# Kernel tuning notes

Hardware: AMD Instinct MI355X
Metric: run time of the kernel (lower is better)

## Reference

```python
import jax, jax.numpy as jnp
import numpy as np
import math

BATCH, T, D_INNER, D_STATE, K = 2, 1024, 1024, 16, 4


def setup_inputs() -> dict:
    key = jax.random.key(0)
    ks = jax.random.split(key, 6)
    x = jax.random.normal(ks[0], (BATCH, T, D_INNER), jnp.float32)
    conv_w = jax.random.normal(ks[1], (D_INNER, 1, K), jnp.float32) * (1.0 / math.sqrt(K))
    conv_b = jax.random.normal(ks[2], (D_INNER,), jnp.float32) * 0.02
    x_proj_w = jax.random.normal(ks[3], (2 * D_STATE, D_INNER), jnp.float32) * (1.0 / math.sqrt(D_INNER))
    dt_proj_w = jax.random.normal(ks[4], (D_INNER, D_STATE), jnp.float32) * (1.0 / math.sqrt(D_STATE))
    dt_proj_b = jax.random.uniform(ks[5], (D_INNER,), jnp.float32, minval=math.log(0.001), maxval=math.log(0.1))
    D = jnp.ones((D_INNER,), jnp.float32)
    return {"x": x, "conv_w": conv_w, "conv_b": conv_b, "x_proj_w": x_proj_w,
            "dt_proj_w": dt_proj_w, "dt_proj_b": dt_proj_b, "D": D}


def _ssm_forward(x, conv_w, conv_b, x_proj_w, dt_proj_w, dt_proj_b, D):
    B_batch, T_len, d_inner = x.shape
    d_state = dt_proj_w.shape[1]
    k = conv_w.shape[-1]
    # Causal depthwise conv1d: torch pads (k-1) both sides then slices [:T] == left-pad (k-1), VALID.
    xp = jnp.pad(x.transpose(0, 2, 1), ((0, 0), (0, 0), (k - 1, 0)))  # (B, d_inner, T+k-1)
    xc = jax.lax.conv_general_dilated(
        xp, conv_w, window_strides=(1,), padding='VALID',
        dimension_numbers=('NCH', 'OIH', 'NCH'), feature_group_count=d_inner)
    xc = xc + conv_b[None, :, None]
    xc = jax.nn.silu(xc).transpose(0, 2, 1)  # (B, T, d_inner)

    proj = jnp.einsum('btd,pd->btp', xc, x_proj_w)  # (B, T, 2*d_state)
    B_ssm, C_ssm = jnp.split(proj, 2, axis=-1)      # each (B, T, d_state)

    # NOTE: original applies softplus twice (once in forward, once in selective_scan).
    dt = jax.nn.softplus(jnp.einsum('bts,ds->btd', B_ssm, dt_proj_w) + dt_proj_b)
    dt = jax.nn.softplus(dt)  # (B, T, d_inner)

    # A = -exp(log(arange(1..d_state))) = -[1..d_state], same for every d_inner channel.
    A = -jnp.arange(1, d_state + 1, dtype=x.dtype)  # (d_state,)

    dA = jnp.exp(dt[..., None] * A)                                  # (B, T, d_inner, d_state)
    dBx = dt[..., None] * B_ssm[:, :, None, :] * xc[..., None]       # (B, T, d_inner, d_state)

    flat = d_inner * d_state
    EPS = 1e-38
    log_dA = jnp.log(jnp.clip(dA, EPS)).reshape(B_batch, T_len, flat)
    log_dBx = jnp.log(jnp.clip(dBx, EPS)).reshape(B_batch, T_len, flat)

    # parallel_scan_log: h_t = exp(cumsum(log_dA) + logcumsumexp(log_dBx - cumsum(log_dA)))
    a_star = jnp.cumsum(log_dA, axis=1)
    h = jnp.exp(a_star + jax.lax.cumlogsumexp(log_dBx - a_star, axis=1))
    h = h.reshape(B_batch, T_len, d_inner, d_state)

    y = jnp.einsum('bts,btds->btd', C_ssm, h) + D * xc
    return y


def reference(x, conv_w, conv_b, x_proj_w, dt_proj_w, dt_proj_b, D):
    return _ssm_forward(x, conv_w, conv_b, x_proj_w, dt_proj_w, dt_proj_b, D)
```

## Files before the change

### kernel.cpp

```cpp
#include <hip/hip_runtime.h>

#define BATCH 2
#define T_LEN 1024
#define D_IN  1024
#define D_ST  16
#define CHUNKS 32
#define CLEN  32
#define DTILE 64
#define NTILES 1024
#define NRPAIR 1024
#define NCHAIN4 8192

struct ABts {
    float row0[D_IN];
    float row1[D_IN];
    alignas(16) float Bsh[2][D_ST];
};
struct Tile {
    float dt[CLEN][DTILE];
    float xc[CLEN][DTILE];
    alignas(16) float B[CLEN][D_ST];
    alignas(16) float C[CLEN][D_ST];
};

__device__ __forceinline__ float softplus_f(float x) {
    return fmaxf(x, 0.0f) + __logf(1.0f + __expf(-fabsf(x)));
}
__device__ __forceinline__ void ld4(float* dst, const float4* src) {
    float4 v = *src; dst[0] = v.x; dst[1] = v.y; dst[2] = v.z; dst[3] = v.w;
}

__device__ __forceinline__ void phase_ab(
    ABts& ab, int rpair, int tid,
    const float* __restrict__ x, const float* __restrict__ cw,
    const float* __restrict__ cb, const float* __restrict__ xpw,
    const float* __restrict__ dtw, const float* __restrict__ dtb,
    float* __restrict__ xcg, float* __restrict__ dtp,
    float* __restrict__ Bss, float* __restrict__ Css)
{
    const int r0g = rpair * 2;
    const int b   = r0g >> 10;
    const int t   = r0g & 1023;
    const int d0  = tid * 4;
    const float* xb = x + (size_t)b * T_LEN * D_IN + d0;
    const float4 z4 = {0,0,0,0};
    float xm3[4], xm2[4], xm1[4], x00[4], xp1[4], wv[16], bb[4];
    { float4 v = (t>=3) ? *(const float4*)(xb + (size_t)(t-3)*D_IN) : z4;
      xm3[0]=v.x; xm3[1]=v.y; xm3[2]=v.z; xm3[3]=v.w; }
    { float4 v = (t>=2) ? *(const float4*)(xb + (size_t)(t-2)*D_IN) : z4;
      xm2[0]=v.x; xm2[1]=v.y; xm2[2]=v.z; xm2[3]=v.w; }
    { float4 v = (t>=1) ? *(const float4*)(xb + (size_t)(t-1)*D_IN) : z4;
      xm1[0]=v.x; xm1[1]=v.y; xm1[2]=v.z; xm1[3]=v.w; }
    ld4(x00, (const float4*)(xb + (size_t)t*D_IN));
    ld4(xp1, (const float4*)(xb + (size_t)(t+1)*D_IN));
    #pragma unroll
    for (int q = 0; q < 4; q++) ld4(&wv[q*4], &((const float4*)cw)[tid*4 + q]);
    ld4(bb, &((const float4*)cb)[tid]);

    float o0[4], o1[4];
    #pragma unroll
    for (int q = 0; q < 4; q++) {
        float a0c = fmaf(wv[q*4+0], xm3[q], fmaf(wv[q*4+1], xm2[q],
                    fmaf(wv[q*4+2], xm1[q], fmaf(wv[q*4+3], x00[q], bb[q]))));
        float a1c = fmaf(wv[q*4+0], xm2[q], fmaf(wv[q*4+1], xm1[q],
                    fmaf(wv[q*4+2], x00[q], fmaf(wv[q*4+3], xp1[q], bb[q]))));
        o0[q] = a0c / (1.0f + __expf(-a0c));
        o1[q] = a1c / (1.0f + __expf(-a1c));
    }
    float4 v0 = {o0[0],o0[1],o0[2],o0[3]};
    float4 v1 = {o1[0],o1[1],o1[2],o1[3]};
    ((float4*)(xcg + (size_t)r0g*D_IN))[tid]     = v0;
    ((float4*)(xcg + (size_t)(r0g+1)*D_IN))[tid] = v1;
    ((float4*)ab.row0)[tid] = v0;
    ((float4*)ab.row1)[tid] = v1;
    __syncthreads();

    const int p = tid >> 3, kg = tid & 7;
    const float4* wr = (const float4*)(xpw + (size_t)p * D_IN);
    const float4* r0 = (const float4*)ab.row0;
    const float4* r1 = (const float4*)ab.row1;
    float4 acc0 = z4, acc1 = z4;
    #pragma unroll
    for (int j = 0; j < 32; j++) {
        int idx = kg + j*8;
        float4 w = wr[idx];
        float4 a = r0[idx];
        float4 c = r1[idx];
        acc0.x = fmaf(a.x, w.x, acc0.x); acc0.y = fmaf(a.y, w.y, acc0.y);
        acc0.z = fmaf(a.z, w.z, acc0.z); acc0.w = fmaf(a.w, w.w, acc0.w);
        acc1.x = fmaf(c.x, w.x, acc1.x); acc1.y = fmaf(c.y, w.y, acc1.y);
        acc1.z = fmaf(c.z, w.z, acc1.z); acc1.w = fmaf(c.w, w.w, acc1.w);
    }
    float v0s = (acc0.x + acc0.y) + (acc0.z + acc0.w);
    float v1s = (acc1.x + acc1.y) + (acc1.z + acc1.w);
    v0s += __shfl_xor(v0s, 1); v0s += __shfl_xor(v0s, 2); v0s += __shfl_xor(v0s, 4);
    v1s += __shfl_xor(v1s, 1); v1s += __shfl_xor(v1s, 2); v1s += __shfl_xor(v1s, 4);
    __syncthreads();
    if (kg == 0) {
        if (p < D_ST) {
            Bss[(size_t)r0g*D_ST + p]     = v0s;
            Bss[(size_t)(r0g+1)*D_ST + p] = v1s;
            ab.Bsh[0][p] = v0s;
            ab.Bsh[1][p] = v1s;
        } else {
            Css[(size_t)r0g*D_ST + (p - D_ST)]     = v0s;
            Css[(size_t)(r0g+1)*D_ST + (p - D_ST)] = v1s;
        }
    }
    __syncthreads();

    const float4* B0 = (const float4*)&ab.Bsh[0][0];
    const float4* B1 = (const float4*)&ab.Bsh[1][0];
    float4 b00 = B0[0], b01 = B0[1], b02 = B0[2], b03 = B0[3];
    float4 b10 = B1[0], b11 = B1[1], b12 = B1[2], b13 = B1[3];
    #pragma unroll
    for (int jd = 0; jd < 4; jd++) {
        int d = jd*256 + tid;
        const float4* wd = (const float4*)(dtw + (size_t)d * D_ST);
        float4 q0 = wd[0], q1 = wd[1], q2 = wd[2], q3 = wd[3];
        float bias = dtb[d];
        float z0 = bias, z1 = bias;
        z0 = fmaf(b00.x,q0.x,z0); z0 = fmaf(b00.y,q0.y,z0);
        z0 = fmaf(b00.z,q0.z,z0); z0 = fmaf(b00.w,q0.w,z0);
        z0 = fmaf(b01.x,q1.x,z0); z0 = fmaf(b01.y,q1.y,z0);
        z0 = fmaf(b01.z,q1.z,z0); z0 = fmaf(b01.w,q1.w,z0);
        z0 = fmaf(b02.x,q2.x,z0); z0 = fmaf(b02.y,q2.y,z0);
        z0 = fmaf(b02.z,q2.z,z0); z0 = fmaf(b02.w,q2.w,z0);
        z0 = fmaf(b03.x,q3.x,z0); z0 = fmaf(b03.y,q3.y,z0);
        z0 = fmaf(b03.z,q3.z,z0); z0 = fmaf(b03.w,q3.w,z0);
        z1 = fmaf(b10.x,q0.x,z1); z1 = fmaf(b10.y,q0.y,z1);
        z1 = fmaf(b10.z,q0.z,z1); z1 = fmaf(b10.w,q0.w,z1);
        z1 = fmaf(b11.x,q1.x,z1); z1 = fmaf(b11.y,q1.y,z1);
        z1 = fmaf(b11.z,q1.z,z1); z1 = fmaf(b11.w,q1.w,z1);
        z1 = fmaf(b12.x,q2.x,z1); z1 = fmaf(b12.y,q2.y,z1);
        z1 = fmaf(b12.z,q2.z,z1); z1 = fmaf(b12.w,q2.w,z1);
        z1 = fmaf(b13.x,q3.x,z1); z1 = fmaf(b13.y,q3.y,z1);
        z1 = fmaf(b13.z,q3.z,z1); z1 = fmaf(b13.w,q3.w,z1);
        dtp[(size_t)r0g*D_IN + d]     = softplus_f(softplus_f(z0));
        dtp[(size_t)(r0g+1)*D_IN + d] = softplus_f(softplus_f(z1));
    }
}

__device__ __forceinline__ void stage_tile(
    Tile& tl, int w, int tid,
    const float* __restrict__ dtp, const float* __restrict__ xcg,
    const float* __restrict__ Bss, const float* __restrict__ Css)
{
    const int chunk = w & (CHUNKS-1);
    const int dg = (w >> 5) & 15;
    const int b  = w >> 9;
    const int t0 = chunk*CLEN, d0 = dg*DTILE;
    #pragma unroll
    for (int k = 0; k < 2; k++) {
        int fidx = tid + k*256;
        int ti = fidx >> 4, c4 = fidx & 15;
        size_t g = (size_t)(b*T_LEN + t0 + ti)*D_IN + d0;
        ((float4*)&tl.dt[ti][0])[c4] = ((const float4*)(dtp + g))[c4];
        ((float4*)&tl.xc[ti][0])[c4] = ((const float4*)(xcg + g))[c4];
    }
    if (tid < 128) {
        int ti = tid >> 2, c4 = tid & 3;
        ((float4*)&tl.B[ti][0])[c4] =
            ((const float4*)(Bss + (size_t)(b*T_LEN + t0 + ti)*D_ST))[c4];
    } else {
        int t2 = tid - 128, ti = t2 >> 2, c4 = t2 & 3;
        ((float4*)&tl.C[ti][0])[c4] =
            ((const float4*)(Css + (size_t)(b*T_LEN + t0 + ti)*D_ST))[c4];
    }
}

__device__ __forceinline__ void tile_partials(
    const Tile& tl, int w, int tid, float* __restrict__ Pq, float* __restrict__ Qq)
{
    const int chunk = w & 31, dg = (w>>5)&15, b = w>>9;
    const int d0 = dg*DTILE;
    const int sg = tid & 3, dl = tid >> 2;
    const float a0 = -(float)(sg*4+1), a1 = -(float)(sg*4+2);
    const float a2 = -(float)(sg*4+3), a3 = -(float)(sg*4+4);
    float h0=0,h1=0,h2=0,h3=0,p0=1,p1=1,p2=1,p3=1;
    #pragma unroll 8
    for (int i = 0; i < CLEN; i++) {
        float dt = tl.dt[i][dl], xv = tl.xc[i][dl];
        float4 bv = *((const float4*)&tl.B[i][sg*4]);
        float e0 = fmaxf(__expf(dt*a0), 1e-38f);
        float e1 = fmaxf(__expf(dt*a1), 1e-38f);
        float e2 = fmaxf(__expf(dt*a2), 1e-38f);
        float e3 = fmaxf(__expf(dt*a3), 1e-38f);
        float q0 = fmaxf(dt*bv.x*xv, 1e-38f);
        float q1 = fmaxf(dt*bv.y*xv, 1e-38f);
        float q2 = fmaxf(dt*bv.z*xv, 1e-38f);
        float q3 = fmaxf(dt*bv.w*xv, 1e-38f);
        h0 = fmaf(e0, h0, q0); p0 *= e0;
        h1 = fmaf(e1, h1, q1); p1 *= e1;
        h2 = fmaf(e2, h2, q2); p2 *= e2;
        h3 = fmaf(e3, h3, q3); p3 *= e3;
    }
    int chain = (b*D_IN + d0 + dl)*4 + sg;
    float4 P4 = {p0,p1,p2,p3}, Q4 = {h0,h1,h2,h3};
    ((float4*)Pq)[(size_t)chunk*NCHAIN4 + chain] = P4;
    ((float4*)Qq)[(size_t)chunk*NCHAIN4 + chain] = Q4;
}

__device__ __forceinline__ float4 chunk_prefix(
    int chunk, int chain, const float* __restrict__ Pq, const float* __restrict__ Qq)
{
    const float4* Pp = (const float4*)Pq;
    const float4* Qp = (const float4*)Qq;
    float4 h = {0,0,0,0};
    #pragma unroll 8
    for (int c = 0; c < CHUNKS-1; c++) {
        float4 pp = Pp[(size_t)c*NCHAIN4 + chain];
        float4 qq = Qp[(size_t)c*NCHAIN4 + chain];
        bool v = (c < chunk);
        h.x = v ? fmaf(pp.x, h.x, qq.x) : h.x;
        h.y = v ? fmaf(pp.y, h.y, qq.y) : h.y;
        h.z = v ? fmaf(pp.z, h.z, qq.z) : h.z;
        h.w = v ? fmaf(pp.w, h.w, qq.w) : h.w;
    }
    return h;
}

__device__ __forceinline__ void tile_replay(
    Tile& tl, int w, int tid, float4 h,
    const float* __restrict__ Dw, float* __restrict__ y)
{
    const int chunk = w & 31, dg = (w>>5)&15, b = w>>9;
    const int t0 = chunk*CLEN, d0 = dg*DTILE;
    const int sg = tid & 3, dl = tid >> 2;
    const float a0 = -(float)(sg*4+1), a1 = -(float)(sg*4+2);
    const float a2 = -(float)(sg*4+3), a3 = -(float)(sg*4+4);
    float Dv = Dw[d0 + dl];
    #pragma unroll 8
    for (int i = 0; i < CLEN; i++) {
        float dt = tl.dt[i][dl], xv = tl.xc[i][dl];
        float4 bv = *((const float4*)&tl.B[i][sg*4]);
        float4 cv = *((const float4*)&tl.C[i][sg*4]);
        float e0 = fmaxf(__expf(dt*a0), 1e-38f);
        float e1 = fmaxf(__expf(dt*a1), 1e-38f);
        float e2 = fmaxf(__expf(dt*a2), 1e-38f);
        float e3 = fmaxf(__expf(dt*a3), 1e-38f);
        float q0 = fmaxf(dt*bv.x*xv, 1e-38f);
        float q1 = fmaxf(dt*bv.y*xv, 1e-38f);
        float q2 = fmaxf(dt*bv.z*xv, 1e-38f);
        float q3 = fmaxf(dt*bv.w*xv, 1e-38f);
        h.x = fmaf(e0, h.x, q0);
        h.y = fmaf(e1, h.y, q1);
        h.z = fmaf(e2, h.z, q2);
        h.w = fmaf(e3, h.w, q3);
        float yp = cv.x*h.x;
        yp = fmaf(cv.y, h.y, yp);
        yp = fmaf(cv.z, h.z, yp);
        yp = fmaf(cv.w, h.w, yp);
        yp += __shfl_xor(yp, 1);
        yp += __shfl_xor(yp, 2);
        if (sg == 0) tl.dt[i][dl] = fmaf(Dv, xv, yp);
    }
    __syncthreads();
    #pragma unroll
    for (int k = 0; k < 2; k++) {
        int fidx = tid + k*256;
        int ti = fidx >> 4, c4 = fidx & 15;
        ((float4*)(y + (size_t)(b*T_LEN + t0 + ti)*D_IN + d0))[c4] =
            ((const float4*)&tl.dt[ti][0])[c4];
    }
}

__global__ __launch_bounds__(256) void ab_k(
    const float* __restrict__ x, const float* __restrict__ cw,
    const float* __restrict__ cb, const float* __restrict__ xpw,
    const float* __restrict__ dtw, const float* __restrict__ dtb,
    float* __restrict__ xcg, float* __restrict__ dtp,
    float* __restrict__ Bss, float* __restrict__ Css)
{
    __shared__ ABts ab;
    phase_ab(ab, blockIdx.x, threadIdx.x, x, cw, cb, xpw, dtw, dtb, xcg, dtp, Bss, Css);
}

__global__ __launch_bounds__(256) void c_k(
    const float* __restrict__ dtp, const float* __restrict__ xcg,
    const float* __restrict__ Bss, const float* __restrict__ Css,
    float* __restrict__ Pq, float* __restrict__ Qq)
{
    __shared__ Tile tl;
    stage_tile(tl, blockIdx.x, threadIdx.x, dtp, xcg, Bss, Css);
    __syncthreads();
    tile_partials(tl, blockIdx.x, threadIdx.x, Pq, Qq);
}

__global__ __launch_bounds__(256) void e2_k(
    const float* __restrict__ dtp, const float* __restrict__ xcg,
    const float* __restrict__ Bss, const float* __restrict__ Css,
    const float* __restrict__ Pq, const float* __restrict__ Qq,
    const float* __restrict__ Dw, float* __restrict__ y)
{
    __shared__ Tile tl;
    const int w = blockIdx.x, tid = threadIdx.x;
    stage_tile(tl, w, tid, dtp, xcg, Bss, Css);
    const int chunk = w & 31, dg = (w>>5)&15, b = w>>9;
    const int sg = tid & 3, dl = tid >> 2;
    const int chain = (b*D_IN + dg*DTILE + dl)*4 + sg;
    float4 h = chunk_prefix(chunk, chain, Pq, Qq);
    __syncthreads();
    tile_replay(tl, w, tid, h, Dw, y);
}

extern "C" void kernel_launch(void* const* d_in, const int* in_sizes, int n_in,
                              void* d_out, int out_size, void* d_ws, size_t ws_size,
                              hipStream_t stream) {
    const float* x   = (const float*)d_in[0];
    const float* cw  = (const float*)d_in[1];
    const float* cb  = (const float*)d_in[2];
    const float* xpw = (const float*)d_in[3];
    const float* dtw = (const float*)d_in[4];
    const float* dtb = (const float*)d_in[5];
    const float* Dw  = (const float*)d_in[6];
    float* y = (float*)d_out;

    const size_t NTD = (size_t)BATCH * T_LEN * D_IN;
    const size_t NTS = (size_t)BATCH * T_LEN * D_ST;
    const size_t NPQ = (size_t)NCHAIN4 * CHUNKS * 4;
    const size_t PAD = 1024;

    float* xc  = (float*)d_ws;
    float* dtp = xc  + NTD + PAD;
    float* Bss = dtp + NTD + PAD;
    float* Css = Bss + NTS + PAD;
    float* Pq  = Css + NTS + PAD;
    float* Qq  = Pq  + NPQ + PAD;

    ab_k<<<NRPAIR, 256, 0, stream>>>(x, cw, cb, xpw, dtw, dtb, xc, dtp, Bss, Css);
    c_k<<<NTILES, 256, 0, stream>>>(dtp, xc, Bss, Css, Pq, Qq);
    e2_k<<<NTILES, 256, 0, stream>>>(dtp, xc, Bss, Css, Pq, Qq, Dw, y);
}
```

Baseline: 131.0 us.

## Add mid kernel computing chunk prefix states once; halve ab_k grid

Adds a separate mid_k kernel that runs the cross-chunk recurrence once per chain and stores each chunk's starting state in H0. Previously every e2_k block re-read up to 31 chunks of P/Q partials, so that global traffic grew quadratically with chunk count. The ab_k kernel now processes two row pairs per block with half the blocks. The cost is an extra launch, a serial 32-step kernel with only 32 blocks, and an extra H0 buffer write and read.

```diff
diff --git a/kernel.cpp b/kernel.cpp
--- a/kernel.cpp
+++ b/kernel.cpp
@@ -199,25 +199,6 @@
     float4 P4 = {p0,p1,p2,p3}, Q4 = {h0,h1,h2,h3};
     ((float4*)Pq)[(size_t)chunk*NCHAIN4 + chain] = P4;
     ((float4*)Qq)[(size_t)chunk*NCHAIN4 + chain] = Q4;
-}
-
-__device__ __forceinline__ float4 chunk_prefix(
-    int chunk, int chain, const float* __restrict__ Pq, const float* __restrict__ Qq)
-{
-    const float4* Pp = (const float4*)Pq;
-    const float4* Qp = (const float4*)Qq;
-    float4 h = {0,0,0,0};
-    #pragma unroll 8
-    for (int c = 0; c < CHUNKS-1; c++) {
-        float4 pp = Pp[(size_t)c*NCHAIN4 + chain];
-        float4 qq = Qp[(size_t)c*NCHAIN4 + chain];
-        bool v = (c < chunk);
-        h.x = v ? fmaf(pp.x, h.x, qq.x) : h.x;
-        h.y = v ? fmaf(pp.y, h.y, qq.y) : h.y;
-        h.z = v ? fmaf(pp.z, h.z, qq.z) : h.z;
-        h.w = v ? fmaf(pp.w, h.w, qq.w) : h.w;
-    }
-    return h;
 }
 
 __device__ __forceinline__ void tile_replay(
@@ -273,7 +254,9 @@
     float* __restrict__ Bss, float* __restrict__ Css)
 {
     __shared__ ABts ab;
-    phase_ab(ab, blockIdx.x, threadIdx.x, x, cw, cb, xpw, dtw, dtb, xcg, dtp, Bss, Css);
+    phase_ab(ab, blockIdx.x*2+0, threadIdx.x, x, cw, cb, xpw, dtw, dtb, xcg, dtp, Bss, Css);
+    __syncthreads();
+    phase_ab(ab, blockIdx.x*2+1, threadIdx.x, x, cw, cb, xpw, dtw, dtb, xcg, dtp, Bss, Css);
 }
 
 __global__ __launch_bounds__(256) void c_k(
@@ -287,11 +270,30 @@
     tile_partials(tl, blockIdx.x, threadIdx.x, Pq, Qq);
 }
 
+__global__ __launch_bounds__(256) void mid_k(
+    const float* __restrict__ Pq, const float* __restrict__ Qq, float* __restrict__ H0)
+{
+    int chain = blockIdx.x*256 + threadIdx.x;
+    const float4* Pp = (const float4*)Pq + chain;
+    const float4* Qp = (const float4*)Qq + chain;
+    float4* Op = (float4*)H0 + chain;
+    float4 h = {0,0,0,0};
+    #pragma unroll 8
+    for (int c = 0; c < CHUNKS; c++) {
+        float4 pp = Pp[(size_t)c*NCHAIN4], qq = Qp[(size_t)c*NCHAIN4];
+        Op[(size_t)c*NCHAIN4] = h;
+        h.x = fmaf(pp.x, h.x, qq.x);
+        h.y = fmaf(pp.y, h.y, qq.y);
+        h.z = fmaf(pp.z, h.z, qq.z);
+        h.w = fmaf(pp.w, h.w, qq.w);
+    }
+}
+
 __global__ __launch_bounds__(256) void e2_k(
     const float* __restrict__ dtp, const float* __restrict__ xcg,
     const float* __restrict__ Bss, const float* __restrict__ Css,
-    const float* __restrict__ Pq, const float* __restrict__ Qq,
-    const float* __restrict__ Dw, float* __restrict__ y)
+    const float* __restrict__ H0, const float* __restrict__ Dw,
+    float* __restrict__ y)
 {
     __shared__ Tile tl;
     const int w = blockIdx.x, tid = threadIdx.x;
@@ -299,7 +301,7 @@
     const int chunk = w & 31, dg = (w>>5)&15, b = w>>9;
     const int sg = tid & 3, dl = tid >> 2;
     const int chain = (b*D_IN + dg*DTILE + dl)*4 + sg;
-    float4 h = chunk_prefix(chunk, chain, Pq, Qq);
+    float4 h = ((const float4*)H0)[(size_t)chunk*NCHAIN4 + chain];
     __syncthreads();
     tile_replay(tl, w, tid, h, Dw, y);
 }
@@ -327,8 +329,10 @@
     float* Css = Bss + NTS + PAD;
     float* Pq  = Css + NTS + PAD;
     float* Qq  = Pq  + NPQ + PAD;
-
-    ab_k<<<NRPAIR, 256, 0, stream>>>(x, cw, cb, xpw, dtw, dtb, xc, dtp, Bss, Css);
+    float* H0  = Qq  + NPQ + PAD;
+
+    ab_k<<<NRPAIR/2, 256, 0, stream>>>(x, cw, cb, xpw, dtw, dtb, xc, dtp, Bss, Css);
     c_k<<<NTILES, 256, 0, stream>>>(dtp, xc, Bss, Css, Pq, Qq);
-    e2_k<<<NTILES, 256, 0, stream>>>(dtp, xc, Bss, Css, Pq, Qq, Dw, y);
-}
+    mid_k<<<NCHAIN4/256, 256, 0, stream>>>(Pq, Qq, H0);
+    e2_k<<<NTILES, 256, 0, stream>>>(dtp, xc, Bss, Css, H0, Dw, y);
+}
```

After: 121.0 us. 1.08x faster.
